# Kernel tuning notes

Hardware: AMD Instinct MI355X
Metric: run time of the kernel (lower is better)

## Reference

```python
import jax, jax.numpy as jnp
import numpy as np

R = 12          # resolution (H = W = G); L = R**3 = 1728
HEADS = 12


def setup_inputs() -> dict:
    key = jax.random.key(0)
    k1, k2, k3 = jax.random.split(key, 3)
    B, L, C = 4, R ** 3, 768
    qkv = jax.random.normal(k1, (3, B, L, C), dtype=jnp.float32)
    lepe_w = jax.random.normal(k2, (C, 1, 3, 3, 3), dtype=jnp.float32) * 0.05
    lepe_b = jax.random.normal(k3, (C,), dtype=jnp.float32) * 0.01
    return {"qkv": qkv, "lepe_w": lepe_w, "lepe_b": lepe_b}


def reference(qkv, lepe_w, lepe_b):
    # qkv: [3, B, L, C]; idx=0 => window == full volume, so attention is dense over L.
    q, k, v = qkv[0], qkv[1], qkv[2]
    B, L, C = q.shape
    hd = C // HEADS
    scale = hd ** -0.5

    # im2cswin with full-volume window preserves token order: [B, L, C] -> [B, H, L, d]
    qh = q.reshape(B, L, HEADS, hd).transpose(0, 2, 1, 3)
    kh = k.reshape(B, L, HEADS, hd).transpose(0, 2, 1, 3)

    # get_lepe: v -> [B, C, R, R, R], depthwise 3x3x3 conv (groups=C)
    v_img = v.transpose(0, 2, 1).reshape(B, C, R, R, R)
    lepe = jax.lax.conv_general_dilated(
        v_img, lepe_w, window_strides=(1, 1, 1), padding="SAME",
        dimension_numbers=("NCDHW", "OIDHW", "NCDHW"), feature_group_count=C,
    ) + lepe_b[None, :, None, None, None]
    lepe = lepe.reshape(B, HEADS, hd, L).transpose(0, 1, 3, 2)   # [B, H, L, d]
    vh = v_img.reshape(B, HEADS, hd, L).transpose(0, 1, 3, 2)    # [B, H, L, d]

    attn = jax.nn.softmax(jnp.einsum("bhqd,bhkd->bhqk", qh * scale, kh), axis=-1)
    out = jnp.einsum("bhqk,bhkd->bhqd", attn, vh) + lepe          # [B, H, L, d]

    # windows2img with full window is an inverse reshape back to [B, L, C]
    return out.transpose(0, 2, 1, 3).reshape(B, L, C)
```

## Files before the change

kernel.cpp:

```cpp
#include <hip/hip_runtime.h>

#define RR 12
#define LL 1728
#define CC 768
#define HEADS 12
#define HD 64
#define BATCH 4

typedef __attribute__((ext_vector_type(8))) short bf8;
typedef __attribute__((ext_vector_type(4))) float f4;

__device__ inline unsigned short f2bf(float x) {
  unsigned int u = __float_as_uint(x);
  return (unsigned short)((u + 0x7FFFu + ((u >> 16) & 1u)) >> 16);
}
__device__ inline unsigned short f2bfr(float x) {
  return (unsigned short)((__float_as_uint(x) + 0x8000u) >> 16);
}

__device__ inline float fast_exp2(float x) {
#if __has_builtin(__builtin_amdgcn_exp2f)
  return __builtin_amdgcn_exp2f(x);
#else
  return exp2f(x);
#endif
}

__device__ inline void gld16(const unsigned short* g, unsigned short* l) {
  __builtin_amdgcn_global_load_lds((const __attribute__((address_space(1))) unsigned int*)g,
                                   (__attribute__((address_space(3))) unsigned int*)l, 16, 0, 0);
}

#define QSCALE 0.1803368801111244f

__global__ __launch_bounds__(256) void wt_kernel(const float* __restrict__ w,
                                                 float* __restrict__ w_t) {
  const int idx = blockIdx.x * 256 + threadIdx.x;
  const int j = idx / CC;
  const int c = idx % CC;
  w_t[idx] = w[c * 27 + j];
}

__global__ __launch_bounds__(256) void prep_kernel(const float* __restrict__ qkv,
                                                   unsigned short* __restrict__ qb,
                                                   unsigned short* __restrict__ kb,
                                                   unsigned short* __restrict__ vT) {
  __shared__ unsigned short tl[64 * 65];
  const int lt = blockIdx.x;
  const int h = blockIdx.y;
  const int b = blockIdx.z;
  const int t = threadIdx.x;

  {
    const int r0 = t >> 4;
    const int c4 = (t & 15) * 4;
#pragma unroll
    for (int p = 0; p < 4; ++p) {
      const int row = lt * 64 + p * 16 + r0;
      const size_t off = ((size_t)b * LL + row) * CC + h * HD + c4;
      const float4 qv = *(const float4*)(qkv + off);
      ushort4 oq;
      oq.x = f2bf(qv.x * QSCALE); oq.y = f2bf(qv.y * QSCALE);
      oq.z = f2bf(qv.z * QSCALE); oq.w = f2bf(qv.w * QSCALE);
      *(ushort4*)(qb + off) = oq;
      const float4 kv = *(const float4*)(qkv + (size_t)BATCH * LL * CC + off);
      ushort4 ok;
      ok.x = f2bf(kv.x); ok.y = f2bf(kv.y); ok.z = f2bf(kv.z); ok.w = f2bf(kv.w);
      *(ushort4*)(kb + off) = ok;
    }
  }

  const float* vsrc = qkv + ((size_t)(2 * BATCH + b)) * LL * CC;
#pragma unroll
  for (int it = 0; it < 4; ++it) {
    const int idx = it * 256 + t;
    const int lrow = idx >> 4;
    const int c4 = (idx & 15) * 4;
    const float4 vv = *(const float4*)(vsrc + (size_t)(lt * 64 + lrow) * CC + h * HD + c4);
    tl[(c4 + 0) * 65 + lrow] = f2bf(vv.x);
    tl[(c4 + 1) * 65 + lrow] = f2bf(vv.y);
    tl[(c4 + 2) * 65 + lrow] = f2bf(vv.z);
    tl[(c4 + 3) * 65 + lrow] = f2bf(vv.w);
  }
  __syncthreads();
#pragma unroll
  for (int it = 0; it < 4; ++it) {
    const int idx = it * 256 + t;
    const int drow = idx >> 4;
    const int s4 = (idx & 15) * 4;
    const int lb = s4 >> 2;
    ushort4 o;
    o.x = tl[drow * 65 + lb];
    o.y = tl[drow * 65 + 16 + lb];
    o.z = tl[drow * 65 + 32 + lb];
    o.w = tl[drow * 65 + 48 + lb];
    *(ushort4*)(vT + (((size_t)(b * HEADS + h) * HD + drow) * LL) + lt * 64 + s4) = o;
  }
}

__global__ __launch_bounds__(256) void lepe_kernel(const float* __restrict__ qkv,
                                                   const float* __restrict__ w_t,
                                                   const float* __restrict__ bias,
                                                   float* __restrict__ out) {
  const int line = blockIdx.x / 3;
  const int xg = (blockIdx.x % 3) * 4;
  const int z = line / RR;
  const int y = line % RR;
  const int c = blockIdx.y * 256 + threadIdx.x;
  const int b = blockIdx.z;
  const float* vb = qkv + ((size_t)(2 * BATCH + b)) * LL * CC + c;

  const float bv = bias[c];
  float acc[4] = {bv, bv, bv, bv};

#pragma unroll
  for (int dz = -1; dz <= 1; ++dz) {
#pragma unroll
    for (int dy = -1; dy <= 1; ++dy) {
      const int zz = z + dz, yy = y + dy;
      const bool lineok = ((unsigned)zz < RR) & ((unsigned)yy < RR);
      const int base = (zz * RR + yy) * RR;
      float v6[6];
#pragma unroll
      for (int p = 0; p < 6; ++p) {
        const int xx = xg - 1 + p;
        const bool ok = lineok & ((unsigned)xx < RR);
        const int lp = ok ? base + xx : 0;
        const float vv = vb[(size_t)lp * CC];
        v6[p] = ok ? vv : 0.f;
      }
      const int jb = ((dz + 1) * 3 + (dy + 1)) * 3;
      const float wL = w_t[(jb + 0) * CC + c];
      const float wC = w_t[(jb + 1) * CC + c];
      const float wR = w_t[(jb + 2) * CC + c];
#pragma unroll
      for (int i = 0; i < 4; ++i)
        acc[i] += wL * v6[i] + wC * v6[i + 1] + wR * v6[i + 2];
    }
  }

  const size_t obase = ((size_t)b * LL + line * RR + xg) * CC + c;
#pragma unroll
  for (int i = 0; i < 4; ++i) out[obase + (size_t)i * CC] = acc[i];
}

__global__ __launch_bounds__(256) void attn_kernel(const unsigned short* __restrict__ qb,
                                                   const unsigned short* __restrict__ kb,
                                                   const unsigned short* __restrict__ vT,
                                                   float* __restrict__ out) {
  __shared__ unsigned short k_lds[2][64 * 64];
  __shared__ unsigned short v_lds[2][64 * 64];
  __shared__ unsigned short p_lds[4][16 * 72];

  const int qt = blockIdx.x;
  const int h = blockIdx.y;
  const int b = blockIdx.z;
  const int t = threadIdx.x;
  const int lane = t & 63;
  const int wave = t >> 6;
  const int m = lane & 15;
  const int quad = lane >> 4;

  bf8 qf[2];
  {
    const size_t qbase = ((size_t)(b * LL + qt * 64 + wave * 16 + m)) * CC + h * HD;
    qf[0] = *(const bf8*)(qb + qbase + quad * 8);
    qf[1] = *(const bf8*)(qb + qbase + 32 + quad * 8);
  }

  int koff[2], voff[2], ldsb[2];
#pragma unroll
  for (int j = 0; j < 2; ++j) {
    const int cidx = (j * 4 + wave) * 64 + lane;
    const int row = cidx >> 3;
    const int sc = (cidx & 7) ^ (row & 7);
    koff[j] = row * CC + sc * 8;
    voff[j] = row * LL + sc * 8;
    ldsb[j] = (j * 4 + wave) * 512;
  }

  const unsigned short* kgb = kb + (size_t)b * LL * CC + h * HD;
  const unsigned short* vgb = vT + ((size_t)(b * HEADS + h) * HD) * LL;

  gld16(kgb + koff[0], &k_lds[0][ldsb[0]]);
  gld16(kgb + koff[1], &k_lds[0][ldsb[1]]);
  gld16(vgb + voff[0], &v_lds[0][ldsb[0]]);
  gld16(vgb + voff[1], &v_lds[0][ldsb[1]]);

  f4 o_acc[4] = {};
  float psum[4] = {0.f, 0.f, 0.f, 0.f};

#define ATTN_BODY(KT, CUR)                                                              \
  {                                                                                     \
    __syncthreads();            \
    if ((KT) < 26) {                                                                    \
      const size_t ko = (size_t)((KT) + 1) * 64 * CC;                                   \
      const int vo = ((KT) + 1) * 64;                                                   \
      gld16(kgb + ko + koff[0], &k_lds[(CUR) ^ 1][ldsb[0]]);                            \
      gld16(kgb + ko + koff[1], &k_lds[(CUR) ^ 1][ldsb[1]]);                            \
      gld16(vgb + vo + voff[0], &v_lds[(CUR) ^ 1][ldsb[0]]);                            \
      gld16(vgb + vo + voff[1], &v_lds[(CUR) ^ 1][ldsb[1]]);                            \
    }                                                                                   \
    f4 s_acc[4] = {};                                                                   \
    _Pragma("unroll")                                                                   \
    for (int nt = 0; nt < 4; ++nt) {                                                    \
      _Pragma("unroll")                                                                 \
      for (int ks = 0; ks < 2; ++ks) {                                                  \
        const int cc = ((ks * 4 + quad) ^ (m & 7)) * 8;                                 \
        const bf8 kf = *(const bf8*)&k_lds[CUR][(nt * 16 + m) * 64 + cc];               \
        s_acc[nt] = __builtin_amdgcn_mfma_f32_16x16x32_bf16(qf[ks], kf, s_acc[nt], 0, 0, 0); \
      }                                                                                 \
    }                                                                                   \
    _Pragma("unroll")                                                                   \
    for (int r = 0; r < 4; ++r) {                                                       \
      const float p0 = fast_exp2(s_acc[0][r]);                                          \
      const float p1 = fast_exp2(s_acc[1][r]);                                          \
      const float p2 = fast_exp2(s_acc[2][r]);                                          \
      const float p3 = fast_exp2(s_acc[3][r]);                                          \
      psum[r] += (p0 + p1) + (p2 + p3);                                                 \
      ushort4 pk;        \
      pk.x = f2bfr(p0); pk.y = f2bfr(p1); pk.z = f2bfr(p2); pk.w = f2bfr(p3);           \
      *(ushort4*)&p_lds[wave][(quad * 4 + r) * 72 + m * 4] = pk;                        \
    }                                                                                   \
    __asm__ volatile("s_waitcnt lgkmcnt(0)" ::: "memory");      \
    bf8 pf[2];                                                                          \
    _Pragma("unroll")                                                                   \
    for (int ks = 0; ks < 2; ++ks)                                                      \
      pf[ks] = *(const bf8*)&p_lds[wave][m * 72 + ks * 32 + quad * 8];                  \
    _Pragma("unroll")                                                                   \
    for (int nt = 0; nt < 4; ++nt) {                                                    \
      _Pragma("unroll")                                                                 \
      for (int ks = 0; ks < 2; ++ks) {                                                  \
        const int cc = ((ks * 4 + quad) ^ (m & 7)) * 8;                                 \
        const bf8 vf = *(const bf8*)&v_lds[CUR][(nt * 16 + m) * 64 + cc];               \
        o_acc[nt] = __builtin_amdgcn_mfma_f32_16x16x32_bf16(pf[ks], vf, o_acc[nt], 0, 0, 0); \
      }                                                                                 \
    }                                                                                   \
  }

  for (int ktp = 0; ktp < 13; ++ktp) {
    const int kt0 = ktp * 2;
    ATTN_BODY(kt0, 0)
    ATTN_BODY(kt0 + 1, 1)
  }
  ATTN_BODY(26, 0)
#undef ATTN_BODY

#pragma unroll
  for (int r = 0; r < 4; ++r) {
    float s = psum[r];
    s += __shfl_xor(s, 1);
    s += __shfl_xor(s, 2);
    s += __shfl_xor(s, 4);
    s += __shfl_xor(s, 8);
    const float inv = 1.0f / s;
    const int row = qt * 64 + wave * 16 + quad * 4 + r;
    float* op = out + ((size_t)b * LL + row) * CC + h * HD;
#pragma unroll
    for (int nt = 0; nt < 4; ++nt) {
      const int cix = nt * 16 + m;
      op[cix] = op[cix] + o_acc[nt][r] * inv;
    }
  }
}

extern "C" void kernel_launch(void* const* d_in, const int* in_sizes, int n_in,
                              void* d_out, int out_size, void* d_ws, size_t ws_size,
                              hipStream_t stream) {
  (void)in_sizes; (void)n_in; (void)ws_size; (void)out_size;
  const float* qkv = (const float*)d_in[0];
  const float* lepe_w = (const float*)d_in[1];
  const float* lepe_b = (const float*)d_in[2];
  float* out = (float*)d_out;

  const size_t NE = (size_t)BATCH * LL * CC;
  unsigned short* qb = (unsigned short*)d_ws;
  unsigned short* kb = qb + NE;
  unsigned short* vT = kb + NE;
  float* w_t = (float*)((char*)d_ws + 3 * NE * 2);

  wt_kernel<<<dim3(CC * 27 / 256), 256, 0, stream>>>(lepe_w, w_t);
  prep_kernel<<<dim3(27, HEADS, BATCH), 256, 0, stream>>>(qkv, qb, kb, vT);
  lepe_kernel<<<dim3(144 * 3, CC / 256, BATCH), 256, 0, stream>>>(qkv, w_t, lepe_b, out);
  attn_kernel<<<dim3(27, HEADS, BATCH), 256, 0, stream>>>(qb, kb, vT, out);
}
```

Measured before the change: 196.9 us.

## Merge weight transpose, prep and LePE conv into one combined launch

Replaces three kernels (weight transpose, q/k/v bf16 prep, LePE depthwise conv) with one kernel whose block index picks either the LePE role or the prep role. LePE blocks now stage their 256 channels' weights in LDS and keep the 27 taps in registers, so the separate transpose kernel and its workspace buffer go away. This cuts launch overhead and lets the memory-bound prep and conv work run concurrently. The cost is per-block weight staging into 27 KB of LDS, plus the register pressure of holding 27 weights.

```diff
diff --git a/kernel.cpp b/kernel.cpp
--- a/kernel.cpp
+++ b/kernel.cpp
@@ -33,115 +33,128 @@
 
 #define QSCALE 0.1803368801111244f
 
-__global__ __launch_bounds__(256) void wt_kernel(const float* __restrict__ w,
-                                                 float* __restrict__ w_t) {
-  const int idx = blockIdx.x * 256 + threadIdx.x;
-  const int j = idx / CC;
-  const int c = idx % CC;
-  w_t[idx] = w[c * 27 + j];
-}
-
-__global__ __launch_bounds__(256) void prep_kernel(const float* __restrict__ qkv,
-                                                   unsigned short* __restrict__ qb,
-                                                   unsigned short* __restrict__ kb,
-                                                   unsigned short* __restrict__ vT) {
-  __shared__ unsigned short tl[64 * 65];
-  const int lt = blockIdx.x;
-  const int h = blockIdx.y;
-  const int b = blockIdx.z;
+#define NLEPE 5184
+#define NPREP 1296
+
+__global__ __launch_bounds__(256) void combined_kernel(const float* __restrict__ qkv,
+                                                       const float* __restrict__ w,
+                                                       const float* __restrict__ bias,
+                                                       unsigned short* __restrict__ qb,
+                                                       unsigned short* __restrict__ kb,
+                                                       unsigned short* __restrict__ vT,
+                                                       float* __restrict__ out) {
+  __shared__ __align__(16) unsigned char smem[27648];
+  const int bid = blockIdx.x;
   const int t = threadIdx.x;
 
-  {
-    const int r0 = t >> 4;
-    const int c4 = (t & 15) * 4;
-#pragma unroll
-    for (int p = 0; p < 4; ++p) {
-      const int row = lt * 64 + p * 16 + r0;
-      const size_t off = ((size_t)b * LL + row) * CC + h * HD + c4;
-      const float4 qv = *(const float4*)(qkv + off);
-      ushort4 oq;
-      oq.x = f2bf(qv.x * QSCALE); oq.y = f2bf(qv.y * QSCALE);
-      oq.z = f2bf(qv.z * QSCALE); oq.w = f2bf(qv.w * QSCALE);
-      *(ushort4*)(qb + off) = oq;
-      const float4 kv = *(const float4*)(qkv + (size_t)BATCH * LL * CC + off);
-      ushort4 ok;
-      ok.x = f2bf(kv.x); ok.y = f2bf(kv.y); ok.z = f2bf(kv.z); ok.w = f2bf(kv.w);
-      *(ushort4*)(kb + off) = ok;
-    }
-  }
-
-  const float* vsrc = qkv + ((size_t)(2 * BATCH + b)) * LL * CC;
-#pragma unroll
-  for (int it = 0; it < 4; ++it) {
-    const int idx = it * 256 + t;
-    const int lrow = idx >> 4;
-    const int c4 = (idx & 15) * 4;
-    const float4 vv = *(const float4*)(vsrc + (size_t)(lt * 64 + lrow) * CC + h * HD + c4);
-    tl[(c4 + 0) * 65 + lrow] = f2bf(vv.x);
-    tl[(c4 + 1) * 65 + lrow] = f2bf(vv.y);
-    tl[(c4 + 2) * 65 + lrow] = f2bf(vv.z);
-    tl[(c4 + 3) * 65 + lrow] = f2bf(vv.w);
-  }
-  __syncthreads();
-#pragma unroll
-  for (int it = 0; it < 4; ++it) {
-    const int idx = it * 256 + t;
-    const int drow = idx >> 4;
-    const int s4 = (idx & 15) * 4;
-    const int lb = s4 >> 2;
-    ushort4 o;
-    o.x = tl[drow * 65 + lb];
-    o.y = tl[drow * 65 + 16 + lb];
-    o.z = tl[drow * 65 + 32 + lb];
-    o.w = tl[drow * 65 + 48 + lb];
-    *(ushort4*)(vT + (((size_t)(b * HEADS + h) * HD + drow) * LL) + lt * 64 + s4) = o;
-  }
-}
-
-__global__ __launch_bounds__(256) void lepe_kernel(const float* __restrict__ qkv,
-                                                   const float* __restrict__ w_t,
-                                                   const float* __restrict__ bias,
-                                                   float* __restrict__ out) {
-  const int line = blockIdx.x / 3;
-  const int xg = (blockIdx.x % 3) * 4;
-  const int z = line / RR;
-  const int y = line % RR;
-  const int c = blockIdx.y * 256 + threadIdx.x;
-  const int b = blockIdx.z;
-  const float* vb = qkv + ((size_t)(2 * BATCH + b)) * LL * CC + c;
-
-  const float bv = bias[c];
-  float acc[4] = {bv, bv, bv, bv};
-
-#pragma unroll
-  for (int dz = -1; dz <= 1; ++dz) {
-#pragma unroll
-    for (int dy = -1; dy <= 1; ++dy) {
-      const int zz = z + dz, yy = y + dy;
-      const bool lineok = ((unsigned)zz < RR) & ((unsigned)yy < RR);
-      const int base = (zz * RR + yy) * RR;
-      float v6[6];
-#pragma unroll
-      for (int p = 0; p < 6; ++p) {
-        const int xx = xg - 1 + p;
-        const bool ok = lineok & ((unsigned)xx < RR);
-        const int lp = ok ? base + xx : 0;
-        const float vv = vb[(size_t)lp * CC];
-        v6[p] = ok ? vv : 0.f;
+  if (bid < NLEPE) {
+    const int xg = (bid % 3) * 4;
+    const int line = (bid / 3) % 144;
+    const int ct = (bid / 432) % 3;
+    const int b = bid / 1296;
+    const int z = line / RR;
+    const int y = line % RR;
+    const int c0 = ct * 256;
+    const int c = c0 + t;
+    float* w_lds = (float*)smem;
+
+    {
+      const float* wsrc = w + (size_t)c0 * 27;
+#pragma unroll
+      for (int i = 0; i < 7; ++i) {
+        const int idx = i * 256 + t;
+        if (idx < 1728) *(float4*)&w_lds[idx * 4] = *(const float4*)&wsrc[idx * 4];
       }
-      const int jb = ((dz + 1) * 3 + (dy + 1)) * 3;
-      const float wL = w_t[(jb + 0) * CC + c];
-      const float wC = w_t[(jb + 1) * CC + c];
-      const float wR = w_t[(jb + 2) * CC + c];
-#pragma unroll
-      for (int i = 0; i < 4; ++i)
-        acc[i] += wL * v6[i] + wC * v6[i + 1] + wR * v6[i + 2];
-    }
-  }
-
-  const size_t obase = ((size_t)b * LL + line * RR + xg) * CC + c;
-#pragma unroll
-  for (int i = 0; i < 4; ++i) out[obase + (size_t)i * CC] = acc[i];
+    }
+    __syncthreads();
+    float wreg[27];
+#pragma unroll
+    for (int j = 0; j < 27; ++j) wreg[j] = w_lds[t * 27 + j];
+
+    const float* vb = qkv + ((size_t)(2 * BATCH + b)) * LL * CC + c;
+    const float bv = bias[c];
+    float acc[4] = {bv, bv, bv, bv};
+
+#pragma unroll
+    for (int dz = -1; dz <= 1; ++dz) {
+#pragma unroll
+      for (int dy = -1; dy <= 1; ++dy) {
+        const int zz = z + dz, yy = y + dy;
+        const bool lineok = ((unsigned)zz < RR) & ((unsigned)yy < RR);
+        const int base = (zz * RR + yy) * RR;
+        float v6[6];
+#pragma unroll
+        for (int p = 0; p < 6; ++p) {
+          const int xx = xg - 1 + p;
+          const bool ok = lineok & ((unsigned)xx < RR);
+          const int lp = ok ? base + xx : 0;
+          const float vv = vb[(size_t)lp * CC];
+          v6[p] = ok ? vv : 0.f;
+        }
+        const int jb = ((dz + 1) * 3 + (dy + 1)) * 3;
+        const float wL = wreg[jb], wC = wreg[jb + 1], wR = wreg[jb + 2];
+#pragma unroll
+        for (int i = 0; i < 4; ++i)
+          acc[i] += wL * v6[i] + wC * v6[i + 1] + wR * v6[i + 2];
+      }
+    }
+    const size_t obase = ((size_t)b * LL + line * RR + xg) * CC + c;
+#pragma unroll
+    for (int i = 0; i < 4; ++i) out[obase + (size_t)i * CC] = acc[i];
+
+  } else {
+    const int p = bid - NLEPE;
+    const int lt = p % 27;
+    const int h = (p / 27) % HEADS;
+    const int b = p / (27 * HEADS);
+    unsigned short* tl = (unsigned short*)smem;
+
+    {
+      const int r0 = t >> 4;
+      const int c4 = (t & 15) * 4;
+#pragma unroll
+      for (int pi = 0; pi < 4; ++pi) {
+        const int row = lt * 64 + pi * 16 + r0;
+        const size_t off = ((size_t)b * LL + row) * CC + h * HD + c4;
+        const float4 qv = *(const float4*)(qkv + off);
+        ushort4 oq;
+        oq.x = f2bf(qv.x * QSCALE); oq.y = f2bf(qv.y * QSCALE);
+        oq.z = f2bf(qv.z * QSCALE); oq.w = f2bf(qv.w * QSCALE);
+        *(ushort4*)(qb + off) = oq;
+        const float4 kv = *(const float4*)(qkv + (size_t)BATCH * LL * CC + off);
+        ushort4 ok;
+        ok.x = f2bf(kv.x); ok.y = f2bf(kv.y); ok.z = f2bf(kv.z); ok.w = f2bf(kv.w);
+        *(ushort4*)(kb + off) = ok;
+      }
+    }
+
+    const float* vsrc = qkv + ((size_t)(2 * BATCH + b)) * LL * CC;
+#pragma unroll
+    for (int it = 0; it < 4; ++it) {
+      const int idx = it * 256 + t;
+      const int lrow = idx >> 4;
+      const int c4 = (idx & 15) * 4;
+      const float4 vv = *(const float4*)(vsrc + (size_t)(lt * 64 + lrow) * CC + h * HD + c4);
+      tl[(c4 + 0) * 65 + lrow] = f2bf(vv.x);
+      tl[(c4 + 1) * 65 + lrow] = f2bf(vv.y);
+      tl[(c4 + 2) * 65 + lrow] = f2bf(vv.z);
+      tl[(c4 + 3) * 65 + lrow] = f2bf(vv.w);
+    }
+    __syncthreads();
+#pragma unroll
+    for (int it = 0; it < 4; ++it) {
+      const int idx = it * 256 + t;
+      const int drow = idx >> 4;
+      const int s4 = (idx & 15) * 4;
+      const int lb = s4 >> 2;
+      ushort4 o;
+      o.x = tl[drow * 65 + lb];
+      o.y = tl[drow * 65 + 16 + lb];
+      o.z = tl[drow * 65 + 32 + lb];
+      o.w = tl[drow * 65 + 48 + lb];
+      *(ushort4*)(vT + (((size_t)(b * HEADS + h) * HD + drow) * LL) + lt * 64 + s4) = o;
+    }
+  }
 }
 
 __global__ __launch_bounds__(256) void attn_kernel(const unsigned short* __restrict__ qb,
@@ -277,10 +290,7 @@
   unsigned short* qb = (unsigned short*)d_ws;
   unsigned short* kb = qb + NE;
   unsigned short* vT = kb + NE;
-  float* w_t = (float*)((char*)d_ws + 3 * NE * 2);
-
-  wt_kernel<<<dim3(CC * 27 / 256), 256, 0, stream>>>(lepe_w, w_t);
-  prep_kernel<<<dim3(27, HEADS, BATCH), 256, 0, stream>>>(qkv, qb, kb, vT);
-  lepe_kernel<<<dim3(144 * 3, CC / 256, BATCH), 256, 0, stream>>>(qkv, w_t, lepe_b, out);
+
+  combined_kernel<<<dim3(NLEPE + NPREP), 256, 0, stream>>>(qkv, lepe_w, lepe_b, qb, kb, vT, out);
   attn_kernel<<<dim3(27, HEADS, BATCH), 256, 0, stream>>>(qb, kb, vT, out);
 }
```

After: 192.6 us. 1.02x faster.
